# Optimization experiments

Hardware: AMD Instinct MI355X
Metric: run time of the kernel (lower is better)

## Reference

```python
import jax, jax.numpy as jnp
import numpy as np

EMBED_DIM = 2048
NUM_Q_HEADS = 16
NUM_KV_HEADS = 4
HEAD_DIM = EMBED_DIM // NUM_Q_HEADS  # 128
N_REP = NUM_Q_HEADS // NUM_KV_HEADS  # 4


def setup_inputs() -> dict:
    key = jax.random.key(0)
    ks = jax.random.split(key, 8)
    B, T, C = 2, 2048, EMBED_DIM
    s = 0.02
    return {
        "x": jax.random.normal(ks[0], (B, T, C), dtype=jnp.float32),
        "Wq": jax.random.normal(ks[1], (C, NUM_Q_HEADS * HEAD_DIM), dtype=jnp.float32) * s,
        "bq": jax.random.normal(ks[2], (NUM_Q_HEADS * HEAD_DIM,), dtype=jnp.float32) * s,
        "Wk": jax.random.normal(ks[3], (C, NUM_KV_HEADS * HEAD_DIM), dtype=jnp.float32) * s,
        "bk": jax.random.normal(ks[4], (NUM_KV_HEADS * HEAD_DIM,), dtype=jnp.float32) * s,
        "Wv": jax.random.normal(ks[5], (C, NUM_KV_HEADS * HEAD_DIM), dtype=jnp.float32) * s,
        "bv": jax.random.normal(ks[6], (NUM_KV_HEADS * HEAD_DIM,), dtype=jnp.float32) * s,
        "Wo": jax.random.normal(ks[7], (C, C), dtype=jnp.float32) * s,
    }


def reference(x, Wq, bq, Wk, bk, Wv, bv, Wo):
    B, T, C = x.shape
    # Projections (torch Linear with bias; weights stored as [in, out])
    q = (x @ Wq + bq).reshape(B, T, NUM_KV_HEADS, N_REP, HEAD_DIM)
    k = (x @ Wk + bk).reshape(B, T, NUM_KV_HEADS, HEAD_DIM)
    v = (x @ Wv + bv).reshape(B, T, NUM_KV_HEADS, HEAD_DIM)
    # GQA: group query heads per kv head instead of materializing repeated K/V.
    # q: [B, G, n_rep, Tq, d], k/v: [B, G, Tk, d]
    q = q.transpose(0, 2, 3, 1, 4)  # B, G, n_rep, T, d
    k = k.transpose(0, 2, 1, 3)     # B, G, T, d
    v = v.transpose(0, 2, 1, 3)
    scale = 1.0 / jnp.sqrt(jnp.asarray(HEAD_DIM, dtype=x.dtype))
    scores = jnp.einsum('bgnqd,bgkd->bgnqk', q, k) * scale
    attn = jax.nn.softmax(scores, axis=-1)
    out = jnp.einsum('bgnqk,bgkd->bgnqd', attn, v)  # B, G, n_rep, T, d
    # merge heads back: (G, n_rep) -> Hq, then [B, T, C]
    out = out.transpose(0, 3, 1, 2, 4).reshape(B, T, C)
    return out @ Wo
```

## Files before the change

kernel.cpp:

```cpp
#include <hip/hip_runtime.h>
#include <hip/hip_bf16.h>
#include <cstdint>
#include <cstddef>

typedef __bf16 bf16;
typedef __attribute__((ext_vector_type(8))) __bf16 bf16x8;
typedef __attribute__((ext_vector_type(4))) __bf16 bf16x4;
typedef __attribute__((ext_vector_type(4))) float f32x4;
typedef __attribute__((ext_vector_type(16))) float f32x16;

#define KPAD 136
#define VPAD 72

__device__ __forceinline__ void async16(const void* g, void* l) {
  __builtin_amdgcn_global_load_lds(
      (const __attribute__((address_space(1))) void*)g,
      (__attribute__((address_space(3))) void*)l,
      16, 0, 0);
}

__device__ __forceinline__ void tr_cvt32(const float* __restrict__ in,
                                         bf16* __restrict__ out, int R, int C,
                                         int bx, int by, float (*ts)[33]) {
  const int tx = threadIdx.x & 31, ty = threadIdx.x >> 5;
  const int c0 = bx * 32, r0 = by * 32;
#pragma unroll
  for (int i = 0; i < 4; ++i)
    ts[ty + i * 8][tx] = in[(size_t)(r0 + ty + i * 8) * C + c0 + tx];
  __syncthreads();
#pragma unroll
  for (int i = 0; i < 4; ++i)
    out[(size_t)(c0 + ty + i * 8) * R + r0 + tx] = (bf16)ts[tx][ty + i * 8];
}

__global__ void prep(const float* __restrict__ x, bf16* __restrict__ xb,
                     const float* __restrict__ Wq, const float* __restrict__ Wk,
                     const float* __restrict__ Wv, const float* __restrict__ Wo,
                     bf16* __restrict__ wqkvT, bf16* __restrict__ woT,
                     const float* __restrict__ bq, const float* __restrict__ bk,
                     const float* __restrict__ bv, bf16* __restrict__ biasq) {
  __shared__ float ts[32][33];
  const int id = blockIdx.x;
  if (id < 4096) {
    int i = id * 256 + threadIdx.x;
    const float* src = x + (size_t)i * 8;
    float4 f0 = *reinterpret_cast<const float4*>(src);
    float4 f1 = *reinterpret_cast<const float4*>(src + 4);
    bf16x8 v = {(bf16)f0.x, (bf16)f0.y, (bf16)f0.z, (bf16)f0.w,
                (bf16)f1.x, (bf16)f1.y, (bf16)f1.z, (bf16)f1.w};
    *reinterpret_cast<bf16x8*>(xb + (size_t)i * 8) = v;
  } else if (id < 8192) {
    int t = id - 4096;
    tr_cvt32(Wq, wqkvT, 2048, 2048, t & 63, t >> 6, ts);
  } else if (id < 9216) {
    int t = id - 8192;
    tr_cvt32(Wk, wqkvT + 2048 * 2048, 2048, 512, t & 15, t >> 4, ts);
  } else if (id < 10240) {
    int t = id - 9216;
    tr_cvt32(Wv, wqkvT + 2560 * 2048, 2048, 512, t & 15, t >> 4, ts);
  } else if (id < 14336) {
    int t = id - 10240;
    tr_cvt32(Wo, woT, 2048, 2048, t & 63, t >> 6, ts);
  } else {
    int i = (id - 14336) * 256 + threadIdx.x;
    float v;
    if (i < 2048) v = bq[i];
    else if (i < 2560) v = bk[i - 2048];
    else v = bv[i - 2560];
    biasq[i] = (bf16)v;
  }
}

template <typename CT, bool HAS_BIAS, bool V_FUSE>
__global__ __launch_bounds__(256, 2)
void gemm_bt(const bf16* __restrict__ A, const bf16* __restrict__ Bt,
             const bf16* __restrict__ bias, CT* __restrict__ C,
             bf16* __restrict__ vt, int M, int N, int K) {
  __shared__ bf16 smem[4][128 * 64];
  const int tid = threadIdx.x;
  const int wave = tid >> 6, lane = tid & 63;
  const int l31 = lane & 31, half = lane >> 5;
  const int row0 = blockIdx.y * 128;
  const int col0 = blockIdx.x * 128;
  const int wm = wave & 1, wn = wave >> 1;
  const int sw = l31 & 7;

  f32x16 acc[2][2];
#pragma unroll
  for (int i = 0; i < 2; ++i)
#pragma unroll
    for (int j = 0; j < 2; ++j)
#pragma unroll
      for (int r = 0; r < 16; ++r) acc[i][j][r] = 0.f;

#define STAGE(buf, k0)                                                         \
  {                                                                            \
    _Pragma("unroll")                                                          \
    for (int j = 0; j < 4; ++j) {                                              \
      int c = tid + j * 256;                                                   \
      int r = c >> 3;                                                          \
      int gs = (c & 7) ^ (r & 7);                                              \
      async16(A + (size_t)(row0 + r) * K + (k0) + gs * 8, &smem[(buf)*2][c * 8]);   \
      async16(Bt + (size_t)(col0 + r) * K + (k0) + gs * 8, &smem[(buf)*2 + 1][c * 8]); \
    }                                                                          \
  }

  STAGE(0, 0);
  __syncthreads();

  const int nt = K >> 6;
  for (int t = 0; t < nt; ++t) {
    const int cur = t & 1;
    if (t + 1 < nt) STAGE(cur ^ 1, (t + 1) << 6);

    const bf16* As = smem[cur * 2];
    const bf16* Bs = smem[cur * 2 + 1];
    bf16x8 a[2][4], b[2][4];
#pragma unroll
    for (int mi = 0; mi < 2; ++mi) {
      int ra = wm * 64 + mi * 32 + l31;
      int rb = wn * 64 + mi * 32 + l31;
#pragma unroll
      for (int ks = 0; ks < 4; ++ks) {
        int pg = (ks * 2 + half) ^ sw;
        a[mi][ks] = *reinterpret_cast<const bf16x8*>(&As[ra * 64 + pg * 8]);
        b[mi][ks] = *reinterpret_cast<const bf16x8*>(&Bs[rb * 64 + pg * 8]);
      }
    }
#pragma unroll
    for (int ks = 0; ks < 4; ++ks)
#pragma unroll
      for (int mi = 0; mi < 2; ++mi)
#pragma unroll
        for (int ni = 0; ni < 2; ++ni)
          acc[mi][ni] = __builtin_amdgcn_mfma_f32_32x32x16_bf16(a[mi][ks], b[ni][ks],
                                                                acc[mi][ni], 0, 0, 0);

    __syncthreads();
  }
#undef STAGE

  if (V_FUSE && col0 >= 2560) {
    bf16* Ls = (bf16*)smem;
#pragma unroll
    for (int mi = 0; mi < 2; ++mi) {
#pragma unroll
      for (int ni = 0; ni < 2; ++ni) {
        int nl = wn * 64 + ni * 32 + l31;
        float bv = HAS_BIAS ? (float)bias[col0 + nl] : 0.f;
#pragma unroll
        for (int r = 0; r < 16; ++r) {
          int ml = wm * 64 + mi * 32 + (r & 3) + 8 * (r >> 2) + 4 * half;
          Ls[nl * 132 + ml] = (bf16)(acc[mi][ni][r] + bv);
        }
      }
    }
    __syncthreads();
    const int bb = row0 >> 11;
    const int t0 = row0 & 2047;
    const int g = (col0 - 2560) >> 7;
    bf16* vbase = vt + (size_t)(bb * 4 + g) * 128 * 2048;
#pragma unroll
    for (int j = 0; j < 16; ++j) {
      int c = tid + j * 256;
      int nl = c >> 5, ml4 = (c & 31) * 4;
      bf16x4 v4 = *reinterpret_cast<const bf16x4*>(&Ls[nl * 132 + ml4]);
      *reinterpret_cast<bf16x4*>(vbase + (size_t)nl * 2048 + t0 + ml4) = v4;
    }
  } else {
#pragma unroll
    for (int mi = 0; mi < 2; ++mi) {
#pragma unroll
      for (int ni = 0; ni < 2; ++ni) {
        int n = col0 + wn * 64 + ni * 32 + l31;
        float bv = HAS_BIAS ? (float)bias[n] : 0.f;
#pragma unroll
        for (int r = 0; r < 16; ++r) {
          int m = row0 + wm * 64 + mi * 32 + (r & 3) + 8 * (r >> 2) + 4 * half;
          C[(size_t)m * N + n] = (CT)(acc[mi][ni][r] + bv);
        }
      }
    }
  }
}

__global__ __launch_bounds__(256, 2)
void attn_kernel(const bf16* __restrict__ QKV, const bf16* __restrict__ Vt,
                 bf16* __restrict__ Out) {
  const int bid = blockIdx.x;
  const int qt = bid & 15;
  const int bh = bid >> 4;
  const int b = bh >> 4, h = bh & 15, g = h >> 2;
  const int tid = threadIdx.x;
  const int wave = tid >> 6, lane = tid & 63;
  const int l31 = lane & 31, half = lane >> 5;

  __shared__ bf16 smem[17920];
  bf16* Ks  = smem;
  bf16* Vts = smem + 8704;
  bf16* Qstage = smem;

  const bf16* Qbase = QKV + ((size_t)b * 2048 + qt * 128) * 3072 + h * 128;
#pragma unroll
  for (int j = 0; j < 8; ++j) {
    int c = tid + j * 256;
    *reinterpret_cast<bf16x8*>(&Qstage[(c >> 4) * KPAD + (c & 15) * 8]) =
        *reinterpret_cast<const bf16x8*>(Qbase + (size_t)(c >> 4) * 3072 + (c & 15) * 8);
  }
  __syncthreads();
  bf16x8 qf[8];
#pragma unroll
  for (int ks = 0; ks < 8; ++ks)
    qf[ks] = *reinterpret_cast<const bf16x8*>(
        &Qstage[(wave * 32 + l31) * KPAD + ks * 16 + half * 8]);

  const bf16* Kbase = QKV + (size_t)b * 2048 * 3072 + 2048 + g * 128;
  const bf16* Vbase = Vt + (size_t)(b * 4 + g) * 128 * 2048;

  f32x16 po[4];
#pragma unroll
  for (int j = 0; j < 4; ++j)
#pragma unroll
    for (int r = 0; r < 16; ++r) po[j][r] = 0.f;
  float lsum = 0.f;
  const float sc = 0.08838834764831845f;

  for (int t0 = 0; t0 < 2048; t0 += 64) {
    __syncthreads();
#pragma unroll
    for (int j = 0; j < 4; ++j) {
      int c = tid + j * 256;
      *reinterpret_cast<bf16x8*>(&Ks[(c >> 4) * KPAD + (c & 15) * 8]) =
          *reinterpret_cast<const bf16x8*>(Kbase + (size_t)(t0 + (c >> 4)) * 3072 + (c & 15) * 8);
      *reinterpret_cast<bf16x8*>(&Vts[(c >> 3) * VPAD + (c & 7) * 8]) =
          *reinterpret_cast<const bf16x8*>(Vbase + (size_t)(c >> 3) * 2048 + t0 + (c & 7) * 8);
    }
    __syncthreads();

    f32x16 s[2];
#pragma unroll
    for (int nt = 0; nt < 2; ++nt)
#pragma unroll
      for (int r = 0; r < 16; ++r) s[nt][r] = 0.f;
#pragma unroll
    for (int ks = 0; ks < 8; ++ks) {
#pragma unroll
      for (int nt = 0; nt < 2; ++nt) {
        bf16x8 kf = *reinterpret_cast<const bf16x8*>(
            &Ks[(nt * 32 + l31) * KPAD + ks * 16 + half * 8]);
        s[nt] = __builtin_amdgcn_mfma_f32_32x32x16_bf16(kf, qf[ks], s[nt], 0, 0, 0);
      }
    }

#pragma unroll
    for (int nt = 0; nt < 2; ++nt)
#pragma unroll
      for (int r = 0; r < 16; ++r) {
        float p = __expf(s[nt][r] * sc);
        lsum += p;
        s[nt][r] = p;
      }

#pragma unroll
    for (int ks2 = 0; ks2 < 4; ++ks2) {
      const int nt = ks2 >> 1;
      const int a = (ks2 & 1) * 8;
      uint32_t x0, x1, x2, x3;
      asm("v_cvt_pk_bf16_f32 %0, %1, %2" : "=v"(x0) : "v"(s[nt][a + 0]), "v"(s[nt][a + 1]));
      asm("v_cvt_pk_bf16_f32 %0, %1, %2" : "=v"(x1) : "v"(s[nt][a + 2]), "v"(s[nt][a + 3]));
      asm("v_cvt_pk_bf16_f32 %0, %1, %2" : "=v"(x2) : "v"(s[nt][a + 4]), "v"(s[nt][a + 5]));
      asm("v_cvt_pk_bf16_f32 %0, %1, %2" : "=v"(x3) : "v"(s[nt][a + 6]), "v"(s[nt][a + 7]));
      asm("v_permlane32_swap_b32 %0, %1" : "+v"(x0), "+v"(x2));
      asm("v_permlane32_swap_b32 %0, %1" : "+v"(x1), "+v"(x3));
      union { uint32_t u[4]; bf16x8 v; } pu;
      pu.u[0] = x0; pu.u[1] = x1; pu.u[2] = x2; pu.u[3] = x3;
      const bf16x8 pf = pu.v;
#pragma unroll
      for (int nd = 0; nd < 4; ++nd) {
        bf16x8 vf = *reinterpret_cast<const bf16x8*>(
            &Vts[(nd * 32 + l31) * VPAD + ks2 * 16 + half * 8]);
        po[nd] = __builtin_amdgcn_mfma_f32_32x32x16_bf16(pf, vf, po[nd], 0, 0, 0);
      }
    }
  }

  float l = lsum + __shfl_xor(lsum, 32, 64);
  float inv = 1.0f / l;

  const size_t qrow0 = (size_t)b * 2048 + (size_t)qt * 128 + wave * 32;
#pragma unroll
  for (int r = 0; r < 16; ++r) {
    int row = (r & 3) + 8 * (r >> 2) + 4 * half;
    float invr = __shfl(inv, row, 64);
#pragma unroll
    for (int nt = 0; nt < 4; ++nt)
      Out[(qrow0 + row) * 2048 + h * 128 + nt * 32 + l31] = (bf16)(po[nt][r] * invr);
  }
}

extern "C" void kernel_launch(void* const* d_in, const int* in_sizes, int n_in,
                              void* d_out, int out_size, void* d_ws, size_t ws_size,
                              hipStream_t stream) {
  const float* x  = (const float*)d_in[0];
  const float* Wq = (const float*)d_in[1];
  const float* bq = (const float*)d_in[2];
  const float* Wk = (const float*)d_in[3];
  const float* bk = (const float*)d_in[4];
  const float* Wv = (const float*)d_in[5];
  const float* bv = (const float*)d_in[6];
  const float* Wo = (const float*)d_in[7];
  float* out = (float*)d_out;
  bf16* ws = (bf16*)d_ws;

  bf16* wqkvT = ws;
  bf16* biasq = ws + 6291456;
  bf16* woT   = ws + 6294528;
  bf16* qkv   = ws + 10488832;
  bf16* vt    = ws + 23071744;
  bf16* aout  = ws + 25168896;
  bf16* xb    = ws + 33557504;

  prep<<<14348, 256, 0, stream>>>(x, xb, Wq, Wk, Wv, Wo, wqkvT, woT,
                                  bq, bk, bv, biasq);

  gemm_bt<bf16, true, true><<<dim3(24, 32), 256, 0, stream>>>(
      xb, wqkvT, biasq, qkv, vt, 4096, 3072, 2048);

  attn_kernel<<<512, 256, 0, stream>>>(qkv, vt, aout);

  gemm_bt<float, false, false><<<dim3(16, 32), 256, 0, stream>>>(
      aout, woT, nullptr, out, nullptr, 4096, 2048, 2048);
}
```

Baseline: 291.9 us.

## Single-buffer GEMM shared memory and raise occupancy to four blocks per CU

Replaces the double-buffered async load pipeline in the bf16 GEMM with a single shared buffer that is loaded and then consumed each k-step between two barriers. Fragments are now loaded just in time per k-slice instead of all at once. This cuts LDS use from 64KB to about 33KB and lowers register pressure, which allows launch bounds of four blocks per CU. The cost is that global-to-LDS loads no longer overlap with MFMA work inside a block, so latency hiding must come from the other resident blocks.

```diff
diff --git a/kernel.cpp b/kernel.cpp
--- a/kernel.cpp
+++ b/kernel.cpp
@@ -72,11 +72,11 @@
 }
 
 template <typename CT, bool HAS_BIAS, bool V_FUSE>
-__global__ __launch_bounds__(256, 2)
+__global__ __launch_bounds__(256, 4)
 void gemm_bt(const bf16* __restrict__ A, const bf16* __restrict__ Bt,
              const bf16* __restrict__ bias, CT* __restrict__ C,
              bf16* __restrict__ vt, int M, int N, int K) {
-  __shared__ bf16 smem[4][128 * 64];
+  __shared__ bf16 smem[16896];
   const int tid = threadIdx.x;
   const int wave = tid >> 6, lane = tid & 63;
   const int l31 = lane & 31, half = lane >> 5;
@@ -93,55 +93,36 @@
 #pragma unroll
       for (int r = 0; r < 16; ++r) acc[i][j][r] = 0.f;
 
-#define STAGE(buf, k0)                                                         \
-  {                                                                            \
-    _Pragma("unroll")                                                          \
-    for (int j = 0; j < 4; ++j) {                                              \
-      int c = tid + j * 256;                                                   \
-      int r = c >> 3;                                                          \
-      int gs = (c & 7) ^ (r & 7);                                              \
-      async16(A + (size_t)(row0 + r) * K + (k0) + gs * 8, &smem[(buf)*2][c * 8]);   \
-      async16(Bt + (size_t)(col0 + r) * K + (k0) + gs * 8, &smem[(buf)*2 + 1][c * 8]); \
-    }                                                                          \
-  }
-
-  STAGE(0, 0);
-  __syncthreads();
-
   const int nt = K >> 6;
   for (int t = 0; t < nt; ++t) {
-    const int cur = t & 1;
-    if (t + 1 < nt) STAGE(cur ^ 1, (t + 1) << 6);
-
-    const bf16* As = smem[cur * 2];
-    const bf16* Bs = smem[cur * 2 + 1];
-    bf16x8 a[2][4], b[2][4];
-#pragma unroll
-    for (int mi = 0; mi < 2; ++mi) {
-      int ra = wm * 64 + mi * 32 + l31;
-      int rb = wn * 64 + mi * 32 + l31;
-#pragma unroll
-      for (int ks = 0; ks < 4; ++ks) {
-        int pg = (ks * 2 + half) ^ sw;
-        a[mi][ks] = *reinterpret_cast<const bf16x8*>(&As[ra * 64 + pg * 8]);
-        b[mi][ks] = *reinterpret_cast<const bf16x8*>(&Bs[rb * 64 + pg * 8]);
-      }
-    }
-#pragma unroll
-    for (int ks = 0; ks < 4; ++ks)
-#pragma unroll
-      for (int mi = 0; mi < 2; ++mi)
-#pragma unroll
-        for (int ni = 0; ni < 2; ++ni)
-          acc[mi][ni] = __builtin_amdgcn_mfma_f32_32x32x16_bf16(a[mi][ks], b[ni][ks],
-                                                                acc[mi][ni], 0, 0, 0);
-
-    __syncthreads();
-  }
-#undef STAGE
+    __syncthreads();
+#pragma unroll
+    for (int j = 0; j < 4; ++j) {
+      int c = tid + j * 256;
+      int r = c >> 3;
+      int gs = (c & 7) ^ (r & 7);
+      async16(A + (size_t)(row0 + r) * K + (t << 6) + gs * 8, &smem[c * 8]);
+      async16(Bt + (size_t)(col0 + r) * K + (t << 6) + gs * 8, &smem[8192 + c * 8]);
+    }
+    __syncthreads();
+
+#pragma unroll
+    for (int ks = 0; ks < 4; ++ks) {
+      int pg = (ks * 2 + half) ^ sw;
+      bf16x8 a0 = *reinterpret_cast<const bf16x8*>(&smem[(wm * 64 + l31) * 64 + pg * 8]);
+      bf16x8 a1 = *reinterpret_cast<const bf16x8*>(&smem[(wm * 64 + 32 + l31) * 64 + pg * 8]);
+      bf16x8 b0 = *reinterpret_cast<const bf16x8*>(&smem[8192 + (wn * 64 + l31) * 64 + pg * 8]);
+      bf16x8 b1 = *reinterpret_cast<const bf16x8*>(&smem[8192 + (wn * 64 + 32 + l31) * 64 + pg * 8]);
+      acc[0][0] = __builtin_amdgcn_mfma_f32_32x32x16_bf16(a0, b0, acc[0][0], 0, 0, 0);
+      acc[0][1] = __builtin_amdgcn_mfma_f32_32x32x16_bf16(a0, b1, acc[0][1], 0, 0, 0);
+      acc[1][0] = __builtin_amdgcn_mfma_f32_32x32x16_bf16(a1, b0, acc[1][0], 0, 0, 0);
+      acc[1][1] = __builtin_amdgcn_mfma_f32_32x32x16_bf16(a1, b1, acc[1][1], 0, 0, 0);
+    }
+  }
 
   if (V_FUSE && col0 >= 2560) {
-    bf16* Ls = (bf16*)smem;
+    __syncthreads();
+    bf16* Ls = smem;
 #pragma unroll
     for (int mi = 0; mi < 2; ++mi) {
 #pragma unroll
```

Measured after the change: 294.6 us. Within noise of the previous version (+0.9%).
